# Optimization experiments

Measured on AMD Instinct MI355X. Metric: run time of the kernel, lower is better.

Reference implementation:

```python
import jax, jax.numpy as jnp
import numpy as np

H, D = 4, 32
EMB = H * D  # 128
COUNTS = [30000, 20000, 25000, 50000]  # pesticide, disease, plant, event
EDGE_TYPES = [(0, 1), (1, 0), (2, 1), (1, 2), (3, 0), (0, 3), (3, 2), (2, 3)]
E = 200000
INV_SQRT_D = 1.0 / float(np.sqrt(D))


def layer_norm(x, g, b, eps=1e-5):
    m = x.mean(-1, keepdims=True)
    v = ((x - m) ** 2).mean(-1, keepdims=True)
    return (x - m) * jax.lax.rsqrt(v + eps) * g + b


def hgt_block(xs, edges, kqvW, kqvb, outW, outb, skip, a_rel, m_rel, p_rel, ln_g, ln_b):
    # type-specific K/Q/V projections -> [N, H, D]
    K, Q, V = [], [], []
    for t in range(4):
        kqv = jnp.einsum('nc,kdc->knd', xs[t], kqvW[t]) + kqvb[t][:, None, :]
        K.append(kqv[0].reshape(-1, H, D))
        Q.append(kqv[1].reshape(-1, H, D))
        V.append(kqv[2].reshape(-1, H, D))
    per_dst = {t: [] for t in range(4)}
    for r, (s, t) in enumerate(EDGE_TYPES):
        src, dst = edges[r, 0], edges[r, 1]
        k_rel = jnp.einsum('ehd,hdf->ehf', K[s][src], a_rel[r])  # relation-specific key transform
        v_rel = jnp.einsum('ehd,hdf->ehf', V[s][src], m_rel[r])  # relation-specific message transform
        logit = (k_rel * Q[t][dst]).sum(-1) * p_rel[r] * INV_SQRT_D  # [E, H]
        per_dst[t].append((logit, v_rel, dst))
    outs = []
    for t in range(4):
        N = xs[t].shape[0]
        logits = jnp.concatenate([p[0] for p in per_dst[t]], axis=0)
        vals = jnp.concatenate([p[1] for p in per_dst[t]], axis=0)
        idx = jnp.concatenate([p[2] for p in per_dst[t]], axis=0)
        # single segment softmax per destination node across ALL incoming edge types (PyG HGTConv)
        mx = jax.ops.segment_max(logits, idx, num_segments=N)
        ex = jnp.exp(logits - mx[idx])
        den = jax.ops.segment_sum(ex, idx, num_segments=N)
        alpha = ex / jnp.maximum(den[idx], 1e-16)
        agg = jax.ops.segment_sum(vals * alpha[..., None], idx, num_segments=N).reshape(N, EMB)
        o = jax.nn.gelu(agg, approximate=False) @ outW[t].T + outb[t]
        sg = jax.nn.sigmoid(skip[t])
        o = sg * o + (1.0 - sg) * xs[t]  # HGTConv learnable skip
        # HGTBlock: residual add, LayerNorm, ReLU (dropout = identity in eval)
        outs.append(jax.nn.relu(layer_norm(o + xs[t], ln_g, ln_b)))
    return outs


def fusion(seq, inW, inb, outW, outb, g, b):
    # seq: [N, 3, EMB]; torch MultiheadAttention self-attention, then mean + LN
    qkv = seq @ inW.T + inb  # [N, 3, 3*EMB]
    q, k, v = jnp.split(qkv, 3, axis=-1)
    heads = lambda x: x.reshape(x.shape[0], 3, H, D).transpose(0, 2, 1, 3)  # [N,H,3,D]
    q, k, v = heads(q), heads(k), heads(v)
    att = jax.nn.softmax(jnp.einsum('nhqd,nhkd->nhqk', q, k) * INV_SQRT_D, axis=-1)
    o = jnp.einsum('nhqk,nhkd->nhqd', att, v).transpose(0, 2, 1, 3).reshape(-1, 3, EMB)
    o = o @ outW.T + outb
    return layer_norm(o.mean(axis=1), g, b)


def _forward(x_pest, x_dis, x_plant, edges, proj_W, proj_b, event_emb, kqv_W, kqv_b,
             out_W, out_b, skip, a_rel, m_rel, p_rel, blk_ln_g, blk_ln_b,
             fin_W, fin_b, fout_W, fout_b, f_ln_g, f_ln_b):
    xs = [jax.nn.relu(x_pest @ proj_W[0].T + proj_b[0]),
          jax.nn.relu(x_dis @ proj_W[1].T + proj_b[1]),
          jax.nn.relu(x_plant @ proj_W[2].T + proj_b[2]),
          event_emb]  # event_emb(arange(N)) == the full table
    layers = []
    cur = xs
    for l in range(3):
        cur = hgt_block(cur, edges, kqv_W[l], kqv_b[l], out_W[l], out_b[l], skip[l],
                        a_rel[l], m_rel[l], p_rel[l], blk_ln_g[l], blk_ln_b[l])
        layers.append(cur)
    outs = []
    for j, t in enumerate([0, 1, 2]):  # pesticide, disease, plant
        seq = jnp.stack([layers[0][t], layers[1][t], layers[2][t]], axis=1)
        outs.append(fusion(seq, fin_W[j], fin_b[j], fout_W[j], fout_b[j], f_ln_g[j], f_ln_b[j]))
    return jnp.concatenate(outs, axis=0)  # [30000+20000+25000, 128]


def setup_inputs() -> dict:
    key = jax.random.key(0)
    ks = iter(jax.random.split(key, 64))
    nrm = lambda shape, s=0.05: jax.random.normal(next(ks), shape, dtype=jnp.float32) * s
    rows = []
    for s, t in EDGE_TYPES:
        rows.append(jnp.stack([jax.random.randint(next(ks), (E,), 0, COUNTS[s]),
                               jax.random.randint(next(ks), (E,), 0, COUNTS[t])]))
    return {
        'x_pest': nrm((COUNTS[0], 64), 1.0),
        'x_dis': nrm((COUNTS[1], 64), 1.0),
        'x_plant': nrm((COUNTS[2], 64), 1.0),
        'edges': jnp.stack(rows).astype(jnp.int32),  # [8, 2, E]
        'proj_W': nrm((3, EMB, 64)), 'proj_b': nrm((3, EMB)),
        'event_emb': nrm((COUNTS[3], EMB), 1.0),
        'kqv_W': nrm((3, 4, 3, EMB, EMB)), 'kqv_b': nrm((3, 4, 3, EMB)),
        'out_W': nrm((3, 4, EMB, EMB)), 'out_b': nrm((3, 4, EMB)),
        'skip': nrm((3, 4), 1.0),
        'a_rel': nrm((3, 8, H, D, D), 0.1), 'm_rel': nrm((3, 8, H, D, D), 0.1),
        'p_rel': jnp.ones((3, 8, H), jnp.float32),
        'blk_ln_g': jnp.ones((3, EMB), jnp.float32), 'blk_ln_b': jnp.zeros((3, EMB), jnp.float32),
        'fin_W': nrm((3, 3 * EMB, EMB)), 'fin_b': nrm((3, 3 * EMB)),
        'fout_W': nrm((3, EMB, EMB)), 'fout_b': nrm((3, EMB)),
        'f_ln_g': jnp.ones((3, EMB), jnp.float32), 'f_ln_b': jnp.zeros((3, EMB), jnp.float32),
    }


def reference(x_pest, x_dis, x_plant, edges, proj_W, proj_b, event_emb, kqv_W, kqv_b,
              out_W, out_b, skip, a_rel, m_rel, p_rel, blk_ln_g, blk_ln_b,
              fin_W, fin_b, fout_W, fout_b, f_ln_g, f_ln_b):
    return _forward(x_pest, x_dis, x_plant, edges, proj_W, proj_b, event_emb, kqv_W, kqv_b,
                    out_W, out_b, skip, a_rel, m_rel, p_rel, blk_ln_g, blk_ln_b,
                    fin_W, fin_b, fout_W, fout_b, f_ln_g, f_ln_b)
```

## Files before the change

### kernel.cpp

```cpp
#include <hip/hip_runtime.h>
#include <math.h>

#define E_CNT 200000
typedef unsigned short bfu;
typedef unsigned short u16;
typedef __attribute__((ext_vector_type(8))) short bh8;
typedef __attribute__((ext_vector_type(4))) float f4;

__device__ __forceinline__ float gelu_f(float x) {
    return 0.5f * x * (1.0f + erff(x * 0.70710678118654752f));
}
__device__ __forceinline__ float bf2f(bfu u) { return __uint_as_float(((unsigned)u) << 16); }
__device__ __forceinline__ bfu f2bf(float f) {
    unsigned u = __float_as_uint(f);
    unsigned r = u + 0x7FFFu + ((u >> 16) & 1u);
    return (bfu)(r >> 16);
}
__device__ __forceinline__ int rsrc_of(int r) {
    const int a[8] = {0, 1, 2, 1, 3, 0, 3, 2}; return a[r];
}
__device__ __forceinline__ int rdst_of(int r) {
    const int a[8] = {1, 0, 1, 2, 0, 3, 2, 3}; return a[r];
}
__device__ __forceinline__ int rpoff_of(int r) {
    const int a[9] = {0, 20001, 50002, 70003, 95004, 125005, 175006, 200007, 250008};
    return a[r];
}

__global__ __launch_bounds__(256) void fill_val(float* p, int n, float v) {
    int i = blockIdx.x * 256 + threadIdx.x;
    if (i < n) p[i] = v;
}

__global__ __launch_bounds__(256) void cvt_pack(
    const float* __restrict__ out_W, const float* __restrict__ kqv_W,
    const float* __restrict__ fin_W, const float* __restrict__ fout_W,
    const float* __restrict__ event_emb,
    bfu* __restrict__ OWB, bfu* __restrict__ KWB, bfu* __restrict__ FINWB,
    bfu* __restrict__ FOUTWB, bfu* __restrict__ EVB)
{
    int i = blockIdx.x * 256 + threadIdx.x;
    const float* src; bfu* dst; size_t so, dox;
    if (i < 49152) { src = out_W; dst = OWB; so = (size_t)i * 4; dox = so; }
    else if (i < 98304) {
        int j = i - 49152; int m = j >> 12; int o = (j & 4095) * 4;
        src = kqv_W; dst = KWB;
        so = (size_t)m * 3 * 16384 + o; dox = (size_t)m * 16384 + o;
    }
    else if (i < 135168) { int j = i - 98304; src = fin_W; dst = FINWB; so = (size_t)j * 4; dox = so; }
    else if (i < 147456) { int j = i - 135168; src = fout_W; dst = FOUTWB; so = (size_t)j * 4; dox = so; }
    else if (i < 1747456) { int j = i - 147456; src = event_emb; dst = EVB; so = (size_t)j * 4; dox = so; }
    else return;
    float4 v = *(const float4*)(src + so);
    uint2 u;
    u.x = ((unsigned)f2bf(v.x)) | (((unsigned)f2bf(v.y)) << 16);
    u.y = ((unsigned)f2bf(v.z)) | (((unsigned)f2bf(v.w)) << 16);
    *(uint2*)(dst + dox) = u;
}

__global__ __launch_bounds__(256) void hist_all(const int* __restrict__ edges, int* __restrict__ rp) {
    int i = blockIdx.x * 256 + threadIdx.x;
    if (i >= 8 * E_CNT) return;
    int r = i / E_CNT, e = i - r * E_CNT;
    int d = edges[(size_t)(2 * r + 1) * E_CNT + e];
    atomicAdd(&rp[rpoff_of(r) + d + 1], 1);
}
__global__ __launch_bounds__(1024) void scan_part(int* __restrict__ a, int* __restrict__ part, int n) {
    __shared__ int lds[1024];
    int t = threadIdx.x, i = blockIdx.x * 1024 + t;
    int v = (i < n) ? a[i] : 0;
    lds[t] = v;
    __syncthreads();
    for (int off = 1; off < 1024; off <<= 1) {
        int u = (t >= off) ? lds[t - off] : 0;
        __syncthreads();
        lds[t] += u;
        __syncthreads();
    }
    if (i < n) a[i] = lds[t];
    if (t == 1023) part[blockIdx.x] = lds[1023];
}
__global__ __launch_bounds__(256) void scan_tot(int* __restrict__ part, int nb) {
    __shared__ int lds[256];
    int t = threadIdx.x;
    int v = (t < nb) ? part[t] : 0;
    lds[t] = v;
    __syncthreads();
    for (int off = 1; off < 256; off <<= 1) {
        int u = (t >= off) ? lds[t - off] : 0;
        __syncthreads();
        lds[t] += u;
        __syncthreads();
    }
    if (t < nb) part[t] = lds[t];
}
__global__ __launch_bounds__(1024) void scan_add(int* __restrict__ a, const int* __restrict__ part, int n) {
    int b = blockIdx.x + 1;
    int i = b * 1024 + threadIdx.x;
    if (i < n) a[i] += part[b - 1];
}
__global__ __launch_bounds__(256) void scatter_all(
    const int* __restrict__ edges, const int* __restrict__ RP,
    int* __restrict__ cur, u16* __restrict__ SIDX) {
    int i = blockIdx.x * 256 + threadIdx.x;
    if (i >= 8 * E_CNT) return;
    int r = i / E_CNT, e = i - r * E_CNT;
    int d = edges[(size_t)(2 * r + 1) * E_CNT + e];
    int pos = RP[rpoff_of(r) + d] + atomicAdd(&cur[r * 50000 + d], 1);
    SIDX[pos] = (u16)edges[(size_t)(2 * r) * E_CNT + e];
}

__global__ __launch_bounds__(256) void proj_gemm(
    const float* __restrict__ X, const float* __restrict__ W,
    const float* __restrict__ bias, bfu* __restrict__ Y, int N)
{
    __shared__ __align__(16) float Wt[32][132];
    __shared__ __align__(16) float Xt[32][36];
    const int tid = threadIdx.x;
    const int r0 = blockIdx.x * 32;
    const int rg = tid >> 5, cg = tid & 31;
    float acc[4][4];
    #pragma unroll
    for (int i = 0; i < 4; ++i)
        #pragma unroll
        for (int j = 0; j < 4; ++j) acc[i][j] = 0.f;
    for (int c0 = 0; c0 < 64; c0 += 32) {
        __syncthreads();
        #pragma unroll
        for (int k = 0; k < 4; ++k) {
            int v = tid + k * 256;
            int j = v >> 3, c4 = (v & 7) * 4;
            float4 w = *(const float4*)(W + (size_t)j * 64 + c0 + c4);
            Wt[c4 + 0][j] = w.x; Wt[c4 + 1][j] = w.y;
            Wt[c4 + 2][j] = w.z; Wt[c4 + 3][j] = w.w;
        }
        {
            int rr = tid >> 3, c4 = (tid & 7) * 4;
            int row = r0 + rr;
            float4 x = make_float4(0.f, 0.f, 0.f, 0.f);
            if (row < N) x = *(const float4*)(X + (size_t)row * 64 + c0 + c4);
            Xt[c4 + 0][rr] = x.x; Xt[c4 + 1][rr] = x.y;
            Xt[c4 + 2][rr] = x.z; Xt[c4 + 3][rr] = x.w;
        }
        __syncthreads();
        #pragma unroll
        for (int cc = 0; cc < 32; ++cc) {
            float4 xv = *(const float4*)(&Xt[cc][rg * 4]);
            float4 wv = *(const float4*)(&Wt[cc][cg * 4]);
            #pragma unroll
            for (int i = 0; i < 4; ++i) {
                float xs = (i == 0) ? xv.x : (i == 1) ? xv.y : (i == 2) ? xv.z : xv.w;
                acc[i][0] = fmaf(xs, wv.x, acc[i][0]);
                acc[i][1] = fmaf(xs, wv.y, acc[i][1]);
                acc[i][2] = fmaf(xs, wv.z, acc[i][2]);
                acc[i][3] = fmaf(xs, wv.w, acc[i][3]);
            }
        }
    }
    float4 bv = *(const float4*)(bias + cg * 4);
    #pragma unroll
    for (int ri = 0; ri < 4; ++ri) {
        int row = r0 + rg * 4 + ri;
        if (row >= N) continue;
        float y0 = fmaxf(acc[ri][0] + bv.x, 0.f);
        float y1 = fmaxf(acc[ri][1] + bv.y, 0.f);
        float y2 = fmaxf(acc[ri][2] + bv.z, 0.f);
        float y3 = fmaxf(acc[ri][3] + bv.w, 0.f);
        uint2 u;
        u.x = ((unsigned)f2bf(y0)) | (((unsigned)f2bf(y1)) << 16);
        u.y = ((unsigned)f2bf(y2)) | (((unsigned)f2bf(y3)) << 16);
        *(uint2*)(Y + (size_t)row * 128 + cg * 4) = u;
    }
}

__global__ __launch_bounds__(256) void build_rel(
    const float* __restrict__ kqvW_l, const float* __restrict__ kqvb_l,
    const float* __restrict__ a_l, const float* __restrict__ m_l,
    bfu* __restrict__ WQAB, float* __restrict__ BQA,
    bfu* __restrict__ WVMB, float* __restrict__ BVM)
{
    __shared__ float As[32][33];
    __shared__ float Ws[32][129];
    int tid = threadIdx.x;
    int b = blockIdx.x;
    if (b < 32) {
        int r = b >> 2, h = b & 3;
        int dt = rdst_of(r);
        const float* Wq = kqvW_l + ((size_t)dt * 3 + 1) * 16384;
        const float* bq = kqvb_l + ((size_t)dt * 3 + 1) * 128;
        const float* A = a_l + (size_t)r * 4096 + h * 1024;
        for (int v = tid; v < 1024; v += 256) As[v >> 5][v & 31] = A[v];
        for (int v = tid; v < 4096; v += 256)
            Ws[v >> 7][v & 127] = Wq[(size_t)(h * 32 + (v >> 7)) * 128 + (v & 127)];
        __syncthreads();
        int c = tid & 127, half = tid >> 7;
        for (int d = half; d < 32; d += 2) {
            float acc = 0.f;
            #pragma unroll
            for (int f = 0; f < 32; ++f) acc = fmaf(As[d][f], Ws[f][c], acc);
            WQAB[((size_t)r * 128 + h * 32 + d) * 128 + c] = f2bf(acc);
        }
        if (tid < 32) {
            int d = tid;
            float acc = 0.f;
            #pragma unroll
            for (int f = 0; f < 32; ++f) acc = fmaf(As[d][f], bq[h * 32 + f], acc);
            BQA[(size_t)r * 128 + h * 32 + d] = acc;
        }
    } else {
        int bb2 = b - 32;
        int r = bb2 >> 2, h = bb2 & 3;
        int st = rsrc_of(r);
        const float* Wv = kqvW_l + ((size_t)st * 3 + 2) * 16384;
        const float* bv = kqvb_l + ((size_t)st * 3 + 2) * 128;
        const float* M = m_l + (size_t)r * 4096 + h * 1024;
        for (int v = tid; v < 1024; v += 256) As[v >> 5][v & 31] = M[v];
        for (int v = tid; v < 4096; v += 256)
            Ws[v >> 7][v & 127] = Wv[(size_t)(h * 32 + (v >> 7)) * 128 + (v & 127)];
        __syncthreads();
        int c = tid & 127, half = tid >> 7;
        for (int f = half; f < 32; f += 2) {
            float acc = 0.f;
            #pragma unroll
            for (int d = 0; d < 32; ++d) acc = fmaf(As[d][f], Ws[d][c], acc);
            WVMB[((size_t)r * 128 + h * 32 + f) * 128 + c] = f2bf(acc);
        }
        if (tid < 32) {
            int f = tid;
            float acc = 0.f;
            #pragma unroll
            for (int d = 0; d < 32; ++d) acc = fmaf(As[d][f], bv[h * 32 + d], acc);
            BVM[(size_t)r * 128 + h * 32 + f] = acc;
        }
    }
}

struct GDesc { const bfu* X; const bfu* W; const float* bias; bfu* Y; int N; int ldy; int bend; };
struct GBatch { GDesc d[9]; };

__global__ __launch_bounds__(256) void mgemm_batch(GBatch gb) {
    int b = blockIdx.x;
    int gi = 0;
    #pragma unroll
    for (int k = 0; k < 8; ++k) gi += (b >= gb.d[k].bend) ? 1 : 0;
    const bfu* X = gb.d[0].X; const bfu* W = gb.d[0].W;
    const float* bi = gb.d[0].bias; bfu* Y = gb.d[0].Y;
    int N = gb.d[0].N, ldy = gb.d[0].ldy, bstart = 0;
    #pragma unroll
    for (int k = 1; k < 9; ++k) {
        if (gi == k) {
            X = gb.d[k].X; W = gb.d[k].W; bi = gb.d[k].bias; Y = gb.d[k].Y;
            N = gb.d[k].N; ldy = gb.d[k].ldy; bstart = gb.d[k - 1].bend;
        }
    }
    int bloc = b - bstart;
    const int tid = threadIdx.x;
    const int wave = tid >> 6, lane = tid & 63;
    const int row16 = lane & 15, kgrp = lane >> 4;
    const int r_base = bloc * 128 + wave * 32;
    f4 acc[2][8];
    #pragma unroll
    for (int t = 0; t < 2; ++t)
        #pragma unroll
        for (int n = 0; n < 8; ++n) acc[t][n] = (f4){0.f, 0.f, 0.f, 0.f};
    bh8 az = {0, 0, 0, 0, 0, 0, 0, 0};
    #pragma unroll
    for (int kb = 0; kb < 4; ++kb) {
        int ar0 = r_base + row16, ar1 = r_base + 16 + row16;
        bh8 a0 = az, a1 = az;
        if (ar0 < N) a0 = *(const bh8*)(X + (size_t)ar0 * 128 + kb * 32 + kgrp * 8);
        if (ar1 < N) a1 = *(const bh8*)(X + (size_t)ar1 * 128 + kb * 32 + kgrp * 8);
        #pragma unroll
        for (int n = 0; n < 8; ++n) {
            bh8 bv = *(const bh8*)(W + (size_t)(n * 16 + row16) * 128 + kb * 32 + kgrp * 8);
            acc[0][n] = __builtin_amdgcn_mfma_f32_16x16x32_bf16(a0, bv, acc[0][n], 0, 0, 0);
            acc[1][n] = __builtin_amdgcn_mfma_f32_16x16x32_bf16(a1, bv, acc[1][n], 0, 0, 0);
        }
    }
    #pragma unroll
    for (int t = 0; t < 2; ++t) {
        const int crow0 = r_base + t * 16 + kgrp * 4;
        #pragma unroll
        for (int n = 0; n < 8; ++n) {
            int col = n * 16 + row16;
            float bn = bi[col];
            #pragma unroll
            for (int j = 0; j < 4; ++j) {
                int row = crow0 + j;
                if (row < N) Y[(size_t)row * ldy + col] = f2bf(acc[t][n][j] + bn);
            }
        }
    }
}

__global__ __launch_bounds__(256) void agg_dual(
    const bfu* QAA, const bfu* __restrict__ QAB,
    const bfu* __restrict__ KA, const bfu* __restrict__ VMA,
    const bfu* __restrict__ KB, const bfu* __restrict__ VMB,
    const int* __restrict__ rpA, const int* __restrict__ rpB,
    const u16* __restrict__ sidx,
    const float* __restrict__ prlA, const float* __restrict__ prlB,
    bfu* ACC, int Nn)
{
    int n = blockIdx.x * 2 + (threadIdx.x >> 7);
    if (n >= Nn) return;
    int half = (threadIdx.x >> 6) & 1;
    int l = threadIdx.x & 63;
    int c = half * 64 + l;
    int h = c >> 5;
    const float inv = 0.17677669529663687f;

    float m0 = -3.0e38f, d0 = 0.f, a0 = 0.f;
    float m1 = -3.0e38f, d1 = 0.f, a1 = 0.f;

    {
        float q = bf2f(QAA[(size_t)n * 128 + c]);
        float ph = prlA[h] * inv;
        int i = rpA[n], e1 = rpA[n + 1];
        for (; i + 1 < e1; i += 2) {
            int s0i = sidx[i], s1i = sidx[i + 1];
            float k0 = bf2f(KA[(size_t)s0i * 128 + c]);
            float k1 = bf2f(KA[(size_t)s1i * 128 + c]);
            float v0 = bf2f(VMA[(size_t)s0i * 128 + c]);
            float v1 = bf2f(VMA[(size_t)s1i * 128 + c]);
            float s0 = k0 * q, s1 = k1 * q;
            #pragma unroll
            for (int off = 1; off <= 16; off <<= 1) {
                s0 += __shfl_xor(s0, off);
                s1 += __shfl_xor(s1, off);
            }
            s0 *= ph; s1 *= ph;
            float nm0 = fmaxf(m0, s0);
            float sc0 = __expf(m0 - nm0), w0 = __expf(s0 - nm0);
            d0 = d0 * sc0 + w0; a0 = fmaf(w0, v0, a0 * sc0); m0 = nm0;
            float nm1 = fmaxf(m1, s1);
            float sc1 = __expf(m1 - nm1), w1 = __expf(s1 - nm1);
            d1 = d1 * sc1 + w1; a1 = fmaf(w1, v1, a1 * sc1); m1 = nm1;
        }
        if (i < e1) {
            int si = sidx[i];
            float k0 = bf2f(KA[(size_t)si * 128 + c]);
            float v0 = bf2f(VMA[(size_t)si * 128 + c]);
            float s0 = k0 * q;
            #pragma unroll
            for (int off = 1; off <= 16; off <<= 1) s0 += __shfl_xor(s0, off);
            s0 *= ph;
            float nm0 = fmaxf(m0, s0);
            float sc0 = __expf(m0 - nm0), w0 = __expf(s0 - nm0);
            d0 = d0 * sc0 + w0; a0 = fmaf(w0, v0, a0 * sc0); m0 = nm0;
        }
    }
    {
        float q = bf2f(QAB[(size_t)n * 128 + c]);
        float ph = prlB[h] * inv;
        int i = rpB[n], e1 = rpB[n + 1];
        for (; i + 1 < e1; i += 2) {
            int s0i = sidx[i], s1i = sidx[i + 1];
            float k0 = bf2f(KB[(size_t)s0i * 128 + c]);
            float k1 = bf2f(KB[(size_t)s1i * 128 + c]);
            float v0 = bf2f(VMB[(size_t)s0i * 128 + c]);
            float v1 = bf2f(VMB[(size_t)s1i * 128 + c]);
            float s0 = k0 * q, s1 = k1 * q;
            #pragma unroll
            for (int off = 1; off <= 16; off <<= 1) {
                s0 += __shfl_xor(s0, off);
                s1 += __shfl_xor(s1, off);
            }
            s0 *= ph; s1 *= ph;
            float nm0 = fmaxf(m0, s0);
            float sc0 = __expf(m0 - nm0), w0 = __expf(s0 - nm0);
            d0 = d0 * sc0 + w0; a0 = fmaf(w0, v0, a0 * sc0); m0 = nm0;
            float nm1 = fmaxf(m1, s1);
            float sc1 = __expf(m1 - nm1), w1 = __expf(s1 - nm1);
            d1 = d1 * sc1 + w1; a1 = fmaf(w1, v1, a1 * sc1); m1 = nm1;
        }
        if (i < e1) {
            int si = sidx[i];
            float k0 = bf2f(KB[(size_t)si * 128 + c]);
            float v0 = bf2f(VMB[(size_t)si * 128 + c]);
            float s0 = k0 * q;
            #pragma unroll
            for (int off = 1; off <= 16; off <<= 1) s0 += __shfl_xor(s0, off);
            s0 *= ph;
            float nm0 = fmaxf(m0, s0);
            float sc0 = __expf(m0 - nm0), w0 = __expf(s0 - nm0);
            d0 = d0 * sc0 + w0; a0 = fmaf(w0, v0, a0 * sc0); m0 = nm0;
        }
    }
    float nm = fmaxf(m0, m1);
    float sA = __expf(m0 - nm), sB = __expf(m1 - nm);
    float d = d0 * sA + d1 * sB;
    float a = a0 * sA + a1 * sB;
    float y = gelu_f(a / fmaxf(d, 1e-16f));
    ACC[(size_t)n * 128 + c] = f2bf(y);
}

__global__ __launch_bounds__(256) void mgemm_epi_layer(
    const bfu* __restrict__ A, const bfu* __restrict__ W, const float* __restrict__ bias,
    const bfu* __restrict__ Xr, const float* __restrict__ skp,
    const float* __restrict__ g, const float* __restrict__ bb,
    bfu* __restrict__ Y, int N)
{
    const int tid = threadIdx.x;
    const int wave = tid >> 6, lane = tid & 63;
    const int row16 = lane & 15, kgrp = lane >> 4;
    const int r_base = blockIdx.x * 64 + wave * 16;
    const int arow = r_base + row16;
    f4 acc[8];
    #pragma unroll
    for (int n = 0; n < 8; ++n) acc[n] = (f4){0.f, 0.f, 0.f, 0.f};
    bh8 az = {0, 0, 0, 0, 0, 0, 0, 0};
    #pragma unroll
    for (int kb = 0; kb < 4; ++kb) {
        bh8 a = az;
        if (arow < N) a = *(const bh8*)(A + (size_t)arow * 128 + kb * 32 + kgrp * 8);
        #pragma unroll
        for (int n = 0; n < 8; ++n) {
            bh8 bv = *(const bh8*)(W + (size_t)(n * 16 + row16) * 128 + kb * 32 + kgrp * 8);
            acc[n] = __builtin_amdgcn_mfma_f32_16x16x32_bf16(a, bv, acc[n], 0, 0, 0);
        }
    }
    const int crow0 = r_base + kgrp * 4;
    float sg = 1.f / (1.f + expf(-skp[0]));
    float z[8][4];
    #pragma unroll
    for (int n = 0; n < 8; ++n) {
        float bn = bias[n * 16 + row16];
        #pragma unroll
        for (int j = 0; j < 4; ++j) z[n][j] = acc[n][j] + bn;
    }
    #pragma unroll
    for (int j = 0; j < 4; ++j) {
        int row = crow0 + j;
        if (row >= N) continue;
        #pragma unroll
        for (int n = 0; n < 8; ++n) {
            float xr = bf2f(Xr[(size_t)row * 128 + n * 16 + row16]);
            z[n][j] = sg * z[n][j] + (1.f - sg) * xr + xr;
        }
    }
    float s[4], q[4];
    #pragma unroll
    for (int j = 0; j < 4; ++j) {
        s[j] = 0.f; q[j] = 0.f;
        #pragma unroll
        for (int n = 0; n < 8; ++n) { s[j] += z[n][j]; q[j] += z[n][j] * z[n][j]; }
    }
    #pragma unroll
    for (int off = 1; off <= 8; off <<= 1) {
        #pragma unroll
        for (int j = 0; j < 4; ++j) {
            s[j] += __shfl_xor(s[j], off);
            q[j] += __shfl_xor(q[j], off);
        }
    }
    #pragma unroll
    for (int j = 0; j < 4; ++j) {
        int row = crow0 + j;
        if (row >= N) continue;
        float mean = s[j] * (1.f / 128.f);
        float var = q[j] * (1.f / 128.f) - mean * mean;
        float inv = rsqrtf(var + 1e-5f);
        #pragma unroll
        for (int n = 0; n < 8; ++n) {
            int col = n * 16 + row16;
            float y = (z[n][j] - mean) * inv * g[col] + bb[col];
            Y[(size_t)row * 128 + col] = f2bf(fmaxf(y, 0.f));
        }
    }
}

__global__ __launch_bounds__(256) void mgemm_epi_ln(
    const bfu* __restrict__ X, const bfu* __restrict__ W, const float* __restrict__ bias,
    const float* __restrict__ g, const float* __restrict__ bb,
    float* __restrict__ Y, int N)
{
    const int tid = threadIdx.x;
    const int wave = tid >> 6, lane = tid & 63;
    const int row16 = lane & 15, kgrp = lane >> 4;
    const int r_base = blockIdx.x * 64 + wave * 16;
    const int arow = r_base + row16;
    f4 acc[8];
    #pragma unroll
    for (int n = 0; n < 8; ++n) acc[n] = (f4){0.f, 0.f, 0.f, 0.f};
    bh8 az = {0, 0, 0, 0, 0, 0, 0, 0};
    #pragma unroll
    for (int kb = 0; kb < 4; ++kb) {
        bh8 a = az;
        if (arow < N) a = *(const bh8*)(X + (size_t)arow * 128 + kb * 32 + kgrp * 8);
        #pragma unroll
        for (int n = 0; n < 8; ++n) {
            bh8 bv = *(const bh8*)(W + (size_t)(n * 16 + row16) * 128 + kb * 32 + kgrp * 8);
            acc[n] = __builtin_amdgcn_mfma_f32_16x16x32_bf16(a, bv, acc[n], 0, 0, 0);
        }
    }
    const int crow0 = r_base + kgrp * 4;
    float z[8][4];
    #pragma unroll
    for (int n = 0; n < 8; ++n) {
        float bn = bias[n * 16 + row16];
        #pragma unroll
        for (int j = 0; j < 4; ++j) z[n][j] = acc[n][j] + bn;
    }
    float s[4], q[4];
    #pragma unroll
    for (int j = 0; j < 4; ++j) {
        s[j] = 0.f; q[j] = 0.f;
        #pragma unroll
        for (int n = 0; n < 8; ++n) { s[j] += z[n][j]; q[j] += z[n][j] * z[n][j]; }
    }
    #pragma unroll
    for (int off = 1; off <= 8; off <<= 1) {
        #pragma unroll
        for (int j = 0; j < 4; ++j) {
            s[j] += __shfl_xor(s[j], off);
            q[j] += __shfl_xor(q[j], off);
        }
    }
    #pragma unroll
    for (int j = 0; j < 4; ++j) {
        int row = crow0 + j;
        if (row >= N) continue;
        float mean = s[j] * (1.f / 128.f);
        float var = q[j] * (1.f / 128.f) - mean * mean;
        float inv = rsqrtf(var + 1e-5f);
        #pragma unroll
        for (int n = 0; n < 8; ++n) {
            int col = n * 16 + row16;
            Y[(size_t)row * 128 + col] = (z[n][j] - mean) * inv * g[col] + bb[col];
        }
    }
}

__global__ __launch_bounds__(256) void attn_fuse(
    const bfu* __restrict__ QKV, bfu* __restrict__ OM, int M)
{
    int n = blockIdx.x * 4 + (threadIdx.x >> 6);
    int l = threadIdx.x & 63;
    if (n >= M) return;
    const bfu* base = QKV + (size_t)n * 1152;
    float q[3][2], k[3][2], v[3][2];
    #pragma unroll
    for (int p = 0; p < 3; ++p) {
        q[p][0] = bf2f(base[(0 * 3 + p) * 128 + l]);
        q[p][1] = bf2f(base[(0 * 3 + p) * 128 + l + 64]);
        k[p][0] = bf2f(base[(1 * 3 + p) * 128 + l]);
        k[p][1] = bf2f(base[(1 * 3 + p) * 128 + l + 64]);
        v[p][0] = bf2f(base[(2 * 3 + p) * 128 + l]);
        v[p][1] = bf2f(base[(2 * 3 + p) * 128 + l + 64]);
    }
    float lgA[3][3], lgB[3][3];
    #pragma unroll
    for (int qi = 0; qi < 3; ++qi)
        #pragma unroll
        for (int ki = 0; ki < 3; ++ki) {
            float s0 = q[qi][0] * k[ki][0];
            float s1 = q[qi][1] * k[ki][1];
            #pragma unroll
            for (int off = 1; off <= 16; off <<= 1) {
                s0 += __shfl_xor(s0, off);
                s1 += __shfl_xor(s1, off);
            }
            lgA[qi][ki] = s0 * 0.17677669529663687f;
            lgB[qi][ki] = s1 * 0.17677669529663687f;
        }
    float oA = 0.f, oB = 0.f;
    #pragma unroll
    for (int qi = 0; qi < 3; ++qi) {
        float mA = fmaxf(lgA[qi][0], fmaxf(lgA[qi][1], lgA[qi][2]));
        float e0 = __expf(lgA[qi][0] - mA), e1 = __expf(lgA[qi][1] - mA), e2 = __expf(lgA[qi][2] - mA);
        float rd = 1.f / (e0 + e1 + e2);
        oA += (e0 * v[0][0] + e1 * v[1][0] + e2 * v[2][0]) * rd;
        float mB = fmaxf(lgB[qi][0], fmaxf(lgB[qi][1], lgB[qi][2]));
        float f0 = __expf(lgB[qi][0] - mB), f1 = __expf(lgB[qi][1] - mB), f2 = __expf(lgB[qi][2] - mB);
        float rdB = 1.f / (f0 + f1 + f2);
        oB += (f0 * v[0][1] + f1 * v[1][1] + f2 * v[2][1]) * rdB;
    }
    OM[(size_t)n * 128 + l] = f2bf(oA * (1.f / 3.f));
    OM[(size_t)n * 128 + l + 64] = f2bf(oB * (1.f / 3.f));
}

extern "C" void kernel_launch(void* const* d_in, const int* in_sizes, int n_in,
                              void* d_out, int out_size, void* d_ws, size_t ws_size,
                              hipStream_t stream)
{
    const float* x_pest   = (const float*)d_in[0];
    const float* x_dis    = (const float*)d_in[1];
    const float* x_plant  = (const float*)d_in[2];
    const int*   edges    = (const int*)d_in[3];
    const float* proj_W   = (const float*)d_in[4];
    const float* proj_b   = (const float*)d_in[5];
    const float* event_emb= (const float*)d_in[6];
    const float* kqv_W    = (const float*)d_in[7];
    const float* kqv_b    = (const float*)d_in[8];
    const float* out_W    = (const float*)d_in[9];
    const float* out_b    = (const float*)d_in[10];
    const float* skip     = (const float*)d_in[11];
    const float* a_rel    = (const float*)d_in[12];
    const float* m_rel    = (const float*)d_in[13];
    const float* p_rel    = (const float*)d_in[14];
    const float* blk_ln_g = (const float*)d_in[15];
    const float* blk_ln_b = (const float*)d_in[16];
    const float* fin_W    = (const float*)d_in[17];
    const float* fin_b    = (const float*)d_in[18];
    const float* fout_W   = (const float*)d_in[19];
    const float* fout_b   = (const float*)d_in[20];
    const float* f_ln_g   = (const float*)d_in[21];
    const float* f_ln_b   = (const float*)d_in[22];
    float* out = (float*)d_out;

    static const int NT[4]  = {30000, 20000, 25000, 50000};
    static const int OFF[4] = {0, 30000, 50000, 75000};
    static const int RPOFF[9] = {0, 20001, 50002, 70003, 95004, 125005, 175006, 200007, 250008};
    static const int DG[4][2][2] = { {{1,1},{4,3}}, {{0,0},{2,2}}, {{3,1},{6,3}}, {{5,0},{7,2}} };

    char* wsb = (char*)d_ws;
    size_t ob = 0;
    auto alc = [&](size_t bytes) -> void* {
        void* p = wsb + ob; ob += (bytes + 255) & ~(size_t)255; return p;
    };
    bfu* LK0  = (bfu*)alc((size_t)75000 * 128 * 2);
    bfu* LK1  = (bfu*)alc((size_t)75000 * 128 * 2);
    bfu* POOL = (bfu*)alc((size_t)210000 * 128 * 2);
    bfu* WQAB = (bfu*)alc((size_t)8 * 16384 * 2);
    float* BQA = (float*)alc((size_t)8 * 128 * 4);
    bfu* WVMB = (bfu*)alc((size_t)8 * 16384 * 2);
    float* BVM = (float*)alc((size_t)8 * 128 * 4);
    bfu* KWB  = (bfu*)alc((size_t)12 * 16384 * 2);
    bfu* OWB  = (bfu*)alc((size_t)12 * 16384 * 2);
    bfu* FINWB = (bfu*)alc((size_t)3 * 49152 * 2);
    bfu* FOUTWB = (bfu*)alc((size_t)3 * 16384 * 2);
    int* RP   = (int*)alc((size_t)250008 * 4);
    int* PART = (int*)alc(1024);
    u16* SIDX = (u16*)alc((size_t)8 * E_CNT * 2);
    if (ws_size < ob) {
        fill_val<<<(out_size + 255) / 256, 256, 0, stream>>>(out, out_size, 1e30f);
        return;
    }
    int* CUR = (int*)POOL;
    bfu* QKVf = POOL;
    bfu* OMB  = POOL + (size_t)20000 * 1152;

    bfu* EVB = (bfu*)out;
    bfu* XB  = (bfu*)((char*)out + 12800000);
    bfu* L2F = (bfu*)((char*)out + 19200000);

    cvt_pack<<<(1747456 + 255) / 256, 256, 0, stream>>>(
        out_W, kqv_W, fin_W, fout_W, event_emb, OWB, KWB, FINWB, FOUTWB, EVB);

    hipMemsetAsync(RP, 0, (size_t)250008 * 4, stream);
    const int eg8 = (8 * E_CNT + 255) / 256;
    hist_all<<<eg8, 256, 0, stream>>>(edges, RP);
    scan_part<<<245, 1024, 0, stream>>>(RP, PART, 250008);
    scan_tot<<<1, 256, 0, stream>>>(PART, 245);
    scan_add<<<244, 1024, 0, stream>>>(RP, PART, 250008);
    hipMemsetAsync(CUR, 0, (size_t)8 * 50000 * 4, stream);
    scatter_all<<<eg8, 256, 0, stream>>>(edges, RP, CUR, SIDX);

    const float* xin0[3] = {x_pest, x_dis, x_plant};
    for (int t = 0; t < 3; ++t) {
        proj_gemm<<<(NT[t] + 31) / 32, 256, 0, stream>>>(
            xin0[t], proj_W + (size_t)t * 8192, proj_b + (size_t)t * 128,
            XB + (size_t)OFF[t] * 128, NT[t]);
    }

    auto launch_batch = [&](GDesc* ds, int cnt) {
        GBatch gb;
        int acc = 0;
        for (int i = 0; i < cnt; ++i) {
            gb.d[i] = ds[i];
            acc += (ds[i].N + 127) / 128;
            gb.d[i].bend = acc;
        }
        for (int i = cnt; i < 9; ++i) { gb.d[i] = gb.d[cnt - 1]; gb.d[i].bend = acc; }
        mgemm_batch<<<acc, 256, 0, stream>>>(gb);
    };

    for (int l = 0; l < 3; ++l) {
        const float* kqvW_l = kqv_W + (size_t)l * 12 * 16384;
        const float* kqvb_l = kqv_b + (size_t)l * 12 * 128;
        build_rel<<<64, 256, 0, stream>>>(kqvW_l, kqvb_l,
            a_rel + (size_t)l * 8 * 4096, m_rel + (size_t)l * 8 * 4096,
            WQAB, BQA, WVMB, BVM);

        auto feat_ptr = [&](int tt) -> const bfu* {
            if (tt == 3) return EVB;
            if (l == 0) return XB + (size_t)OFF[tt] * 128;
            return (l == 1 ? LK0 : LK1) + (size_t)OFF[tt] * 128;
        };

        int nord = (l == 2) ? 3 : 4;
        for (int dt = 0; dt < nord; ++dt) {
            int Ndt = NT[dt];
            int rA = DG[dt][0][0], sA = DG[dt][0][1];
            int rB = DG[dt][1][0], sB = DG[dt][1][1];
            int NsA = NT[sA], NsB = NT[sB];
            bfu* QA_A = POOL;
            bfu* QA_B = QA_A + (size_t)Ndt * 128;
            bfu* K_A  = QA_B + (size_t)Ndt * 128;
            bfu* VM_A = K_A + (size_t)NsA * 128;
            bfu* K_B  = VM_A + (size_t)NsA * 128;
            bfu* VM_B = K_B + (size_t)NsB * 128;

            GDesc ds[6];
            ds[0] = { feat_ptr(dt), WQAB + (size_t)rA * 16384, BQA + (size_t)rA * 128, QA_A, Ndt, 128, 0 };
            ds[1] = { feat_ptr(dt), WQAB + (size_t)rB * 16384, BQA + (size_t)rB * 128, QA_B, Ndt, 128, 0 };
            ds[2] = { feat_ptr(sA), KWB + (size_t)(l * 4 + sA) * 16384,
                      kqvb_l + ((size_t)sA * 3 + 0) * 128, K_A, NsA, 128, 0 };
            ds[3] = { feat_ptr(sA), WVMB + (size_t)rA * 16384, BVM + (size_t)rA * 128, VM_A, NsA, 128, 0 };
            ds[4] = { feat_ptr(sB), KWB + (size_t)(l * 4 + sB) * 16384,
                      kqvb_l + ((size_t)sB * 3 + 0) * 128, K_B, NsB, 128, 0 };
            ds[5] = { feat_ptr(sB), WVMB + (size_t)rB * 16384, BVM + (size_t)rB * 128, VM_B, NsB, 128, 0 };
            launch_batch(ds, 6);

            agg_dual<<<(Ndt + 1) / 2, 256, 0, stream>>>(
                QA_A, QA_B, K_A, VM_A, K_B, VM_B,
                RP + RPOFF[rA], RP + RPOFF[rB], SIDX,
                p_rel + (size_t)(l * 8 + rA) * 4, p_rel + (size_t)(l * 8 + rB) * 4,
                QA_A , Ndt);

            size_t wi = (size_t)l * 4 + dt;
            const bfu* xr = feat_ptr(dt);
            bfu* ydst = (dt == 3) ? EVB :
                        (l == 0 ? LK0 : (l == 1 ? LK1 : L2F)) + (size_t)OFF[dt] * 128;
            mgemm_epi_layer<<<(Ndt + 63) / 64, 256, 0, stream>>>(
                QA_A, OWB + wi * 16384, out_b + wi * 128, xr, skip + wi,
                blk_ln_g + (size_t)l * 128, blk_ln_b + (size_t)l * 128, ydst, Ndt);
        }
    }

    const int CH = 20000;
    for (int j = 0; j < 3; ++j) {
        int Nj = NT[j];
        for (int b0 = 0; b0 < Nj; b0 += CH) {
            int M = min(CH, Nj - b0);
            const bfu* srcs[3] = {
                LK0 + (size_t)(OFF[j] + b0) * 128,
                LK1 + (size_t)(OFF[j] + b0) * 128,
                L2F + (size_t)(OFF[j] + b0) * 128 };
            GDesc ds[9];
            int di = 0;
            for (int kk = 0; kk < 3; ++kk)
                for (int p = 0; p < 3; ++p) {
                    ds[di++] = { srcs[p], FINWB + (size_t)j * 49152 + (size_t)kk * 16384,
                                 fin_b + (size_t)j * 384 + kk * 128,
                                 QKVf + (size_t)(kk * 3 + p) * 128, M, 1152, 0 };
                }
            launch_batch(ds, 9);
            attn_fuse<<<(M + 3) / 4, 256, 0, stream>>>(QKVf, OMB, M);
            mgemm_epi_ln<<<(M + 63) / 64, 256, 0, stream>>>(
                OMB, FOUTWB + (size_t)j * 16384, fout_b + (size_t)j * 128,
                f_ln_g + (size_t)j * 128, f_ln_b + (size_t)j * 128,
                out + (size_t)(OFF[j] + b0) * 128, M);
        }
    }
}
```

Before: 2.119 ms.

## Use one wavefront per node with packed bf16x2 loads in aggregation

The aggregation kernel now assigns one 64-lane wavefront per destination node instead of two. Each lane handles two adjacent channels through 32-bit packed bf16 loads and stores, so the per-head reduction needs 4 shuffle steps instead of 5. The two interleaved online-softmax chains are merged into one chain shared by both channels, and the grid is resized to four nodes per block. This halves the number of threads and index loads per edge, at the cost of less parallelism per node and a longer serial dependency chain per lane.

```diff
diff --git a/kernel.cpp b/kernel.cpp
--- a/kernel.cpp
+++ b/kernel.cpp
@@ -302,97 +302,90 @@
     const float* __restrict__ prlA, const float* __restrict__ prlB,
     bfu* ACC, int Nn)
 {
-    int n = blockIdx.x * 2 + (threadIdx.x >> 7);
+    int n = blockIdx.x * 4 + (threadIdx.x >> 6);
     if (n >= Nn) return;
-    int half = (threadIdx.x >> 6) & 1;
     int l = threadIdx.x & 63;
-    int c = half * 64 + l;
-    int h = c >> 5;
-    const float inv = 0.17677669529663687f;
-
-    float m0 = -3.0e38f, d0 = 0.f, a0 = 0.f;
-    float m1 = -3.0e38f, d1 = 0.f, a1 = 0.f;
+    int h = l >> 4;
+    const float scl = 0.17677669529663687f;
+
+    float m = -3.0e38f, d = 0.f, a0 = 0.f, a1 = 0.f;
+
+    auto upd = [&](float s, unsigned vu) {
+        float nm = fmaxf(m, s);
+        float sc = __expf(m - nm), w = __expf(s - nm);
+        d = d * sc + w;
+        a0 = fmaf(w, bf2f((bfu)vu), a0 * sc);
+        a1 = fmaf(w, bf2f((bfu)(vu >> 16)), a1 * sc);
+        m = nm;
+    };
 
     {
-        float q = bf2f(QAA[(size_t)n * 128 + c]);
-        float ph = prlA[h] * inv;
+        unsigned qu = *(const unsigned*)(QAA + (size_t)n * 128 + 2 * l);
+        float q0 = bf2f((bfu)qu), q1 = bf2f((bfu)(qu >> 16));
+        float ph = prlA[h] * scl;
         int i = rpA[n], e1 = rpA[n + 1];
         for (; i + 1 < e1; i += 2) {
-            int s0i = sidx[i], s1i = sidx[i + 1];
-            float k0 = bf2f(KA[(size_t)s0i * 128 + c]);
-            float k1 = bf2f(KA[(size_t)s1i * 128 + c]);
-            float v0 = bf2f(VMA[(size_t)s0i * 128 + c]);
-            float v1 = bf2f(VMA[(size_t)s1i * 128 + c]);
-            float s0 = k0 * q, s1 = k1 * q;
-            #pragma unroll
-            for (int off = 1; off <= 16; off <<= 1) {
+            int sa = sidx[i], sb = sidx[i + 1];
+            unsigned ka = *(const unsigned*)(KA + (size_t)sa * 128 + 2 * l);
+            unsigned kb = *(const unsigned*)(KA + (size_t)sb * 128 + 2 * l);
+            unsigned va = *(const unsigned*)(VMA + (size_t)sa * 128 + 2 * l);
+            unsigned vb = *(const unsigned*)(VMA + (size_t)sb * 128 + 2 * l);
+            float s0 = fmaf(bf2f((bfu)ka), q0, bf2f((bfu)(ka >> 16)) * q1);
+            float s1 = fmaf(bf2f((bfu)kb), q0, bf2f((bfu)(kb >> 16)) * q1);
+            #pragma unroll
+            for (int off = 1; off <= 8; off <<= 1) {
                 s0 += __shfl_xor(s0, off);
                 s1 += __shfl_xor(s1, off);
             }
-            s0 *= ph; s1 *= ph;
-            float nm0 = fmaxf(m0, s0);
-            float sc0 = __expf(m0 - nm0), w0 = __expf(s0 - nm0);
-            d0 = d0 * sc0 + w0; a0 = fmaf(w0, v0, a0 * sc0); m0 = nm0;
-            float nm1 = fmaxf(m1, s1);
-            float sc1 = __expf(m1 - nm1), w1 = __expf(s1 - nm1);
-            d1 = d1 * sc1 + w1; a1 = fmaf(w1, v1, a1 * sc1); m1 = nm1;
+            upd(s0 * ph, va);
+            upd(s1 * ph, vb);
         }
         if (i < e1) {
-            int si = sidx[i];
-            float k0 = bf2f(KA[(size_t)si * 128 + c]);
-            float v0 = bf2f(VMA[(size_t)si * 128 + c]);
-            float s0 = k0 * q;
-            #pragma unroll
-            for (int off = 1; off <= 16; off <<= 1) s0 += __shfl_xor(s0, off);
-            s0 *= ph;
-            float nm0 = fmaxf(m0, s0);
-            float sc0 = __expf(m0 - nm0), w0 = __expf(s0 - nm0);
-            d0 = d0 * sc0 + w0; a0 = fmaf(w0, v0, a0 * sc0); m0 = nm0;
+            int sa = sidx[i];
+            unsigned ka = *(const unsigned*)(KA + (size_t)sa * 128 + 2 * l);
+            unsigned va = *(const unsigned*)(VMA + (size_t)sa * 128 + 2 * l);
+            float s0 = fmaf(bf2f((bfu)ka), q0, bf2f((bfu)(ka >> 16)) * q1);
+            #pragma unroll
+            for (int off = 1; off <= 8; off <<= 1) s0 += __shfl_xor(s0, off);
+            upd(s0 * ph, va);
         }
     }
     {
-        float q = bf2f(QAB[(size_t)n * 128 + c]);
-        float ph = prlB[h] * inv;
+        unsigned qu = *(const unsigned*)(QAB + (size_t)n * 128 + 2 * l);
+        float q0 = bf2f((bfu)qu), q1 = bf2f((bfu)(qu >> 16));
+        float ph = prlB[h] * scl;
         int i = rpB[n], e1 = rpB[n + 1];
         for (; i + 1 < e1; i += 2) {
-            int s0i = sidx[i], s1i = sidx[i + 1];
-            float k0 = bf2f(KB[(size_t)s0i * 128 + c]);
-            float k1 = bf2f(KB[(size_t)s1i * 128 + c]);
-            float v0 = bf2f(VMB[(size_t)s0i * 128 + c]);
-            float v1 = bf2f(VMB[(size_t)s1i * 128 + c]);
-            float s0 = k0 * q, s1 = k1 * q;
-            #pragma unroll
-            for (int off = 1; off <= 16; off <<= 1) {
+            int sa = sidx[i], sb = sidx[i + 1];
+            unsigned ka = *(const unsigned*)(KB + (size_t)sa * 128 + 2 * l);
+            unsigned kb = *(const unsigned*)(KB + (size_t)sb * 128 + 2 * l);
+            unsigned va = *(const unsigned*)(VMB + (size_t)sa * 128 + 2 * l);
+            unsigned vb = *(const unsigned*)(VMB + (size_t)sb * 128 + 2 * l);
+            float s0 = fmaf(bf2f((bfu)ka), q0, bf2f((bfu)(ka >> 16)) * q1);
+            float s1 = fmaf(bf2f((bfu)kb), q0, bf2f((bfu)(kb >> 16)) * q1);
+            #pragma unroll
+            for (int off = 1; off <= 8; off <<= 1) {
                 s0 += __shfl_xor(s0, off);
                 s1 += __shfl_xor(s1, off);
             }
-            s0 *= ph; s1 *= ph;
-            float nm0 = fmaxf(m0, s0);
-            float sc0 = __expf(m0 - nm0), w0 = __expf(s0 - nm0);
-            d0 = d0 * sc0 + w0; a0 = fmaf(w0, v0, a0 * sc0); m0 = nm0;
-            float nm1 = fmaxf(m1, s1);
-            float sc1 = __expf(m1 - nm1), w1 = __expf(s1 - nm1);
-            d1 = d1 * sc1 + w1; a1 = fmaf(w1, v1, a1 * sc1); m1 = nm1;
+            upd(s0 * ph, va);
+            upd(s1 * ph, vb);
         }
         if (i < e1) {
-            int si = sidx[i];
-            float k0 = bf2f(KB[(size_t)si * 128 + c]);
-            float v0 = bf2f(VMB[(size_t)si * 128 + c]);
-            float s0 = k0 * q;
-            #pragma unroll
-            for (int off = 1; off <= 16; off <<= 1) s0 += __shfl_xor(s0, off);
-            s0 *= ph;
-            float nm0 = fmaxf(m0, s0);
-            float sc0 = __expf(m0 - nm0), w0 = __expf(s0 - nm0);
-            d0 = d0 * sc0 + w0; a0 = fmaf(w0, v0, a0 * sc0); m0 = nm0;
-        }
-    }
-    float nm = fmaxf(m0, m1);
-    float sA = __expf(m0 - nm), sB = __expf(m1 - nm);
-    float d = d0 * sA + d1 * sB;
-    float a = a0 * sA + a1 * sB;
-    float y = gelu_f(a / fmaxf(d, 1e-16f));
-    ACC[(size_t)n * 128 + c] = f2bf(y);
+            int sa = sidx[i];
+            unsigned ka = *(const unsigned*)(KB + (size_t)sa * 128 + 2 * l);
+            unsigned va = *(const unsigned*)(VMB + (size_t)sa * 128 + 2 * l);
+            float s0 = fmaf(bf2f((bfu)ka), q0, bf2f((bfu)(ka >> 16)) * q1);
+            #pragma unroll
+            for (int off = 1; off <= 8; off <<= 1) s0 += __shfl_xor(s0, off);
+            upd(s0 * ph, va);
+        }
+    }
+    float rd = 1.f / fmaxf(d, 1e-16f);
+    float y0 = gelu_f(a0 * rd);
+    float y1 = gelu_f(a1 * rd);
+    unsigned ou = ((unsigned)f2bf(y0)) | (((unsigned)f2bf(y1)) << 16);
+    *(unsigned*)(ACC + (size_t)n * 128 + 2 * l) = ou;
 }
 
 __global__ __launch_bounds__(256) void mgemm_epi_layer(
@@ -713,7 +706,7 @@
             ds[5] = { feat_ptr(sB), WVMB + (size_t)rB * 16384, BVM + (size_t)rB * 128, VM_B, NsB, 128, 0 };
             launch_batch(ds, 6);
 
-            agg_dual<<<(Ndt + 1) / 2, 256, 0, stream>>>(
+            agg_dual<<<(Ndt + 3) / 4, 256, 0, stream>>>(
                 QA_A, QA_B, K_A, VM_A, K_B, VM_B,
                 RP + RPOFF[rA], RP + RPOFF[rB], SIDX,
                 p_rel + (size_t)(l * 8 + rA) * 4, p_rel + (size_t)(l * 8 + rB) * 4,
```

Result: faster. 1.802 ms (median of 2 runs) (-15.0%).
